# Kernel optimization log

Hardware: AMD Instinct MI355X
Metric: run time of the kernel (lower is better)

## Reference

```python
import jax, jax.numpy as jnp
import numpy as np

B = 8192
I = 1024  # input_size
H = 1024  # hidden_size


def setup_inputs() -> dict:
    key = jax.random.key(0)
    ks = jax.random.split(key, 8)
    s_i = 1.0 / np.sqrt(I)
    s_h = 1.0 / np.sqrt(H)
    return {
        "x": jax.random.normal(ks[0], (B, I), dtype=jnp.float32),
        "h": jax.random.normal(ks[1], (B, H), dtype=jnp.float32),
        # nn.Linear weights have shape [out, in]; y = x @ W.T
        "W_wz": jax.random.uniform(ks[2], (H, I), jnp.float32, -s_i, s_i),
        "W_uz": jax.random.uniform(ks[3], (H, H), jnp.float32, -s_h, s_h),
        "W_wr": jax.random.uniform(ks[4], (H, I), jnp.float32, -s_i, s_i),
        "W_ur": jax.random.uniform(ks[5], (H, H), jnp.float32, -s_h, s_h),
        "W_u": jax.random.uniform(ks[6], (H, H), jnp.float32, -s_h, s_h),
        "W_w": jax.random.uniform(ks[7], (H, I), jnp.float32, -s_i, s_i),
    }


def reference(x, h, W_wz, W_uz, W_wr, W_ur, W_u, W_w):
    # Fuse the three x-projections and the two h-projections into grouped GEMMs.
    # [B, 3H] = x @ [I, 3H]
    xp = x @ jnp.concatenate([W_wz, W_wr, W_w], axis=0).T
    hp = h @ jnp.concatenate([W_uz, W_ur], axis=0).T  # [B, 2H]
    z = jax.nn.sigmoid(xp[:, :H] + hp[:, :H])
    r = jax.nn.sigmoid(xp[:, H:2 * H] + hp[:, H:])
    h_t = jnp.tanh((r * h) @ W_u.T + xp[:, 2 * H:])
    return z * h + (1.0 - z) * h_t
```

## Files before the change

kernel.cpp:

```cpp
#include <hip/hip_runtime.h>

typedef unsigned short u16;
typedef __attribute__((ext_vector_type(8))) short bf16x8;
typedef __attribute__((ext_vector_type(8))) unsigned short u16x8;
typedef __attribute__((ext_vector_type(4))) float f32x4;

__device__ __forceinline__ u16 f2b(float f) {
  unsigned u = __float_as_uint(f);
  u += 0x7FFFu + ((u >> 16) & 1u);
  return (u16)(u >> 16);
}
__device__ __forceinline__ float sigm(float x) { return 1.0f / (1.0f + __expf(-x)); }
__device__ __forceinline__ float tanh_f(float x) { return 1.0f - 2.0f / (__expf(2.0f * x) + 1.0f); }

__device__ __forceinline__ void cp16(const u16* g, u16* l) {
  __builtin_amdgcn_global_load_lds(
      (const __attribute__((address_space(1))) unsigned int*)g,
      (__attribute__((address_space(3))) unsigned int*)l, 16, 0, 0);
}

__device__ __forceinline__ int swz(int b) {
  return b ^ (((b >> 7) & 3) << 5) ^ (((b >> 9) & 1) << 4);
}

__device__ __forceinline__ u16x8 cvt8(float4 a, float4 b) {
  u16x8 v;
  v[0] = f2b(a.x); v[1] = f2b(a.y); v[2] = f2b(a.z); v[3] = f2b(a.w);
  v[4] = f2b(b.x); v[5] = f2b(b.y); v[6] = f2b(b.z); v[7] = f2b(b.w);
  return v;
}

__global__ __launch_bounds__(256) void pack_xh(const float* __restrict__ x,
                                               const float* __restrict__ h,
                                               u16* __restrict__ xhb,
                                               u16* __restrict__ A2) {
  int idx = blockIdx.x * 256 + threadIdx.x;
  int row = idx >> 8;
  int k = (idx & 255) << 3;
  const float* src = (k < 1024) ? (x + (size_t)row * 1024 + k)
                                : (h + (size_t)row * 1024 + (k - 1024));
  float4 a = *reinterpret_cast<const float4*>(src);
  float4 b = *reinterpret_cast<const float4*>(src + 4);
  u16x8 v = cvt8(a, b);
  *reinterpret_cast<u16x8*>(xhb + ((size_t)row << 11) + k) = v;
  if (k < 1024)
    *reinterpret_cast<u16x8*>(A2 + ((size_t)row << 11) + 1024 + k) = v;
}

__global__ __launch_bounds__(256) void pack_W(const float* __restrict__ Wwz,
                                              const float* __restrict__ Wuz,
                                              const float* __restrict__ Wwr,
                                              const float* __restrict__ Wur,
                                              const float* __restrict__ Wu,
                                              const float* __restrict__ Ww,
                                              u16* __restrict__ W1b,
                                              u16* __restrict__ W2b) {
  int idx = blockIdx.x * 256 + threadIdx.x;
  const float* src;
  u16* dst;
  if (idx < 524288) {
    int row = idx >> 8;
    int k = (idx & 255) << 3;
    const float* lo = (row < 1024) ? Wwz : Wwr;
    const float* hi = (row < 1024) ? Wuz : Wur;
    int n = row & 1023;
    src = (k < 1024) ? (lo + (size_t)n * 1024 + k) : (hi + (size_t)n * 1024 + (k - 1024));
    dst = W1b + ((size_t)row << 11) + k;
  } else {
    int j = idx - 524288;
    int row = j >> 8;
    int k = (j & 255) << 3;
    src = (k < 1024) ? (Wu + (size_t)row * 1024 + k) : (Ww + (size_t)row * 1024 + (k - 1024));
    dst = W2b + ((size_t)row << 11) + k;
  }
  float4 a = *reinterpret_cast<const float4*>(src);
  float4 b = *reinterpret_cast<const float4*>(src + 4);
  *reinterpret_cast<u16x8*>(dst) = cvt8(a, b);
}

__device__ __forceinline__ void body(int t, int NT,
                                     const u16* __restrict__ Ag, const u16* __restrict__ Bg,
                                     int lda, int ldb,
                                     const u16* Ar, const u16* Br, u16* Aw, u16* Bw,
                                     int r0, int c2, int arl0, int arl1,
                                     int wr, int wc, int tid, f32x4 acc[4][4]) {
  const int ab = wr * 4096;
  const int bb = wc * 4096;
  bf16x8 af0[2][2], bfr[4][2];
#pragma unroll
  for (int mm = 0; mm < 2; ++mm) {
    af0[mm][0] = *reinterpret_cast<const bf16x8*>(Ar + ab + mm * 1024 + arl0);
    af0[mm][1] = *reinterpret_cast<const bf16x8*>(Ar + ab + mm * 1024 + arl1);
  }
#pragma unroll
  for (int nf = 0; nf < 4; ++nf) {
    bfr[nf][0] = *reinterpret_cast<const bf16x8*>(Br + bb + nf * 1024 + arl0);
    bfr[nf][1] = *reinterpret_cast<const bf16x8*>(Br + bb + nf * 1024 + arl1);
  }
  if (t + 1 < NT) {
    const u16* g0 = Ag + (size_t)r0 * lda + c2 + (size_t)(t + 1) * 64;
    u16* l0 = Aw + tid * 8;
    cp16(g0, l0); cp16(g0 + (size_t)64 * lda, l0 + 4096);
    const u16* g1 = Ag + (size_t)(128 + r0) * lda + c2 + (size_t)(t + 1) * 64;
    u16* l1 = Aw + 8192 + tid * 8;
    cp16(g1, l1); cp16(g1 + (size_t)64 * lda, l1 + 4096);
  }
  __builtin_amdgcn_s_barrier();
  __builtin_amdgcn_s_setprio(1);
#pragma unroll
  for (int mm = 0; mm < 2; ++mm)
#pragma unroll
    for (int nf = 0; nf < 4; ++nf)
#pragma unroll
      for (int ks = 0; ks < 2; ++ks)
        acc[mm][nf] = __builtin_amdgcn_mfma_f32_16x16x32_bf16(
            af0[mm][ks], bfr[nf][ks], acc[mm][nf], 0, 0, 0);
  __builtin_amdgcn_s_setprio(0);
  __builtin_amdgcn_s_barrier();
  bf16x8 af1[2][2];
#pragma unroll
  for (int mm = 0; mm < 2; ++mm) {
    af1[mm][0] = *reinterpret_cast<const bf16x8*>(Ar + ab + (2 + mm) * 1024 + arl0);
    af1[mm][1] = *reinterpret_cast<const bf16x8*>(Ar + ab + (2 + mm) * 1024 + arl1);
  }
  if (t + 2 < NT) {
    const u16* g = Bg + (size_t)r0 * ldb + c2 + (size_t)(t + 2) * 64;
    u16* l = Bw + tid * 8;
    cp16(g, l); cp16(g + (size_t)64 * ldb, l + 4096);
    asm volatile("s_waitcnt vmcnt(2)" ::: "memory");
  } else {
    asm volatile("s_waitcnt vmcnt(0)" ::: "memory");
  }
  __builtin_amdgcn_s_barrier();
  __builtin_amdgcn_s_setprio(1);
#pragma unroll
  for (int mm = 0; mm < 2; ++mm)
#pragma unroll
    for (int nf = 0; nf < 4; ++nf)
#pragma unroll
      for (int ks = 0; ks < 2; ++ks)
        acc[2 + mm][nf] = __builtin_amdgcn_mfma_f32_16x16x32_bf16(
            af1[mm][ks], bfr[nf][ks], acc[2 + mm][nf], 0, 0, 0);
  __builtin_amdgcn_s_setprio(0);
  __builtin_amdgcn_s_barrier();
}

__device__ __forceinline__ void core(const u16* __restrict__ Ag, const u16* __restrict__ Bg,
                                     int lda, int ldb, int NT,
                                     u16* As0, u16* As1, u16* Bs0, u16* Bs1,
                                     f32x4 acc[4][4]) {
  const int tid = threadIdx.x;
  const int lane = tid & 63;
  const int wid = tid >> 6;
  const int wr = wid >> 1;
  const int wc = wid & 1;

  const int plo = tid * 16;
  const int olo = swz(plo);
  const int r0 = olo >> 7;
  const int c2 = (olo & 127) >> 1;

  const int frow = lane & 15;
  const int fcb = (lane >> 4) * 16;
  const int mask = ((frow & 3) << 5) | (((frow >> 2) & 1) << 4);
  const int arl0 = (frow * 128 + ((fcb + 0) ^ mask)) >> 1;
  const int arl1 = (frow * 128 + ((fcb + 64) ^ mask)) >> 1;

  {
    const u16* g; u16* l;
    g = Ag + (size_t)r0 * lda + c2;          l = As0 + tid * 8;        cp16(g, l); cp16(g + (size_t)64 * lda, l + 4096);
    g = Ag + (size_t)(128 + r0) * lda + c2;  l = As0 + 8192 + tid * 8; cp16(g, l); cp16(g + (size_t)64 * lda, l + 4096);
    g = Bg + (size_t)r0 * ldb + c2;          l = Bs0 + tid * 8;        cp16(g, l); cp16(g + (size_t)64 * ldb, l + 4096);
    g = Bg + (size_t)r0 * ldb + c2 + 64;     l = Bs1 + tid * 8;        cp16(g, l); cp16(g + (size_t)64 * ldb, l + 4096);
  }
  asm volatile("s_waitcnt vmcnt(2)" ::: "memory");
  __builtin_amdgcn_s_barrier();

  for (int u = 0; u < NT; u += 2) {
    body(u,     NT, Ag, Bg, lda, ldb, As0, Bs0, As1, Bs0, r0, c2, arl0, arl1, wr, wc, tid, acc);
    body(u + 1, NT, Ag, Bg, lda, ldb, As1, Bs1, As0, Bs1, r0, c2, arl0, arl1, wr, wc, tid, acc);
  }
}

#define CORE_PRE()                                           \
  __shared__ u16 As0[16384];                                 \
  __shared__ u16 As1[16384];                                 \
  __shared__ u16 Bs0[8192];                                  \
  __shared__ u16 Bs1[8192];                                  \
  f32x4 acc[4][4];                                           \
  _Pragma("unroll") for (int m = 0; m < 4; ++m)              \
  _Pragma("unroll") for (int n = 0; n < 4; ++n)              \
      acc[m][n] = (f32x4){0.f, 0.f, 0.f, 0.f};

__global__ __launch_bounds__(512) void gemm_zr(const u16* __restrict__ xhb,
                                               const u16* __restrict__ W1b,
                                               const float* __restrict__ h,
                                               float* __restrict__ zout,
                                               u16* __restrict__ A2) {
  int b = blockIdx.x;
  int wg = (b & 7) * 64 + (b >> 3);
  int mb = wg >> 4, nb = wg & 15;
  const int m0 = mb * 256, n0 = nb * 128;
  CORE_PRE();
  core(xhb + (size_t)m0 * 2048, W1b + (size_t)n0 * 2048, 2048, 2048, 32,
       As0, As1, Bs0, Bs1, acc);

  const int lane = threadIdx.x & 63;
  const int wid = threadIdx.x >> 6;
  const int wr = wid >> 1, wc = wid & 1;
  const int rbase = m0 + wr * 64 + ((lane >> 4) << 2);
  const int cbase = n0 + wc * 64 + (lane & 15);
  const int isz = (n0 < 1024);
#pragma unroll
  for (int m = 0; m < 4; ++m) {
#pragma unroll
    for (int nf = 0; nf < 4; ++nf) {
      const int col = cbase + nf * 16;
#pragma unroll
      for (int j = 0; j < 4; ++j) {
        const int row = rbase + m * 16 + j;
        const float v = acc[m][nf][j];
        if (isz) {
          zout[(size_t)row * 1024 + col] = sigm(v);
        } else {
          const int c = col - 1024;
          const float rh = sigm(v) * h[(size_t)row * 1024 + c];
          A2[((size_t)row << 11) + c] = f2b(rh);
        }
      }
    }
  }
}

__global__ __launch_bounds__(512) void gemm2_k(const u16* __restrict__ A2,
                                               const u16* __restrict__ W2b,
                                               const float* __restrict__ h,
                                               float* __restrict__ out) {
  int b = blockIdx.x;
  int wg = (b & 7) * 32 + (b >> 3);
  int mb = wg >> 3, nb = wg & 7;
  const int m0 = mb * 256, n0 = nb * 128;
  CORE_PRE();
  core(A2 + (size_t)m0 * 2048, W2b + (size_t)n0 * 2048, 2048, 2048, 32,
       As0, As1, Bs0, Bs1, acc);

  const int lane = threadIdx.x & 63;
  const int wid = threadIdx.x >> 6;
  const int wr = wid >> 1, wc = wid & 1;
  const int rbase = m0 + wr * 64 + ((lane >> 4) << 2);
  const int cbase = n0 + wc * 64 + (lane & 15);
#pragma unroll
  for (int m = 0; m < 4; ++m) {
#pragma unroll
    for (int nf = 0; nf < 4; ++nf) {
      const int col = cbase + nf * 16;
#pragma unroll
      for (int j = 0; j < 4; ++j) {
        const int row = rbase + m * 16 + j;
        const size_t idx = (size_t)row * 1024 + col;
        const float z = out[idx];
        const float hv = h[idx];
        const float ht = tanh_f(acc[m][nf][j]);
        out[idx] = z * hv + (1.0f - z) * ht;
      }
    }
  }
}

extern "C" void kernel_launch(void* const* d_in, const int* in_sizes, int n_in,
                              void* d_out, int out_size, void* d_ws, size_t ws_size,
                              hipStream_t stream) {
  const float* x   = (const float*)d_in[0];
  const float* h   = (const float*)d_in[1];
  const float* Wwz = (const float*)d_in[2];
  const float* Wuz = (const float*)d_in[3];
  const float* Wwr = (const float*)d_in[4];
  const float* Wur = (const float*)d_in[5];
  const float* Wu  = (const float*)d_in[6];
  const float* Ww  = (const float*)d_in[7];
  float* out = (float*)d_out;

  char* ws = (char*)d_ws;
  u16* xhb = (u16*)(ws);
  u16* A2  = (u16*)(ws + 33554432);
  u16* W1b = (u16*)(ws + 67108864);
  u16* W2b = (u16*)(ws + 75497472);

  pack_xh<<<8192, 256, 0, stream>>>(x, h, xhb, A2);
  pack_W<<<3072, 256, 0, stream>>>(Wwz, Wuz, Wwr, Wur, Wu, Ww, W1b, W2b);
  gemm_zr<<<512, 512, 0, stream>>>(xhb, W1b, h, out, A2);
  gemm2_k<<<256, 512, 0, stream>>>(A2, W2b, h, out);
}
```

Measured before the change: 313.0 us.

## Replace swizzled 64-wide K pipeline with simple 32-wide double-buffered loop

The hand-scheduled GEMM main loop is replaced. It had XOR-swizzled LDS layout, split A/B prefetch, manual vmcnt waits and setprio. The new loop uses a simple double buffer with 32-element K tiles and __syncthreads. LDS per block is halved and launch bounds request 4 blocks per CU to raise occupancy. In exchange, the unswizzled 64-byte-row LDS layout may cause bank conflicts, and twice as many barriers run per K.

```diff
diff --git a/kernel.cpp b/kernel.cpp
--- a/kernel.cpp
+++ b/kernel.cpp
@@ -17,10 +17,6 @@
   __builtin_amdgcn_global_load_lds(
       (const __attribute__((address_space(1))) unsigned int*)g,
       (__attribute__((address_space(3))) unsigned int*)l, 16, 0, 0);
-}
-
-__device__ __forceinline__ int swz(int b) {
-  return b ^ (((b >> 7) & 3) << 5) ^ (((b >> 9) & 1) << 4);
 }
 
 __device__ __forceinline__ u16x8 cvt8(float4 a, float4 b) {
@@ -78,71 +74,29 @@
   *reinterpret_cast<u16x8*>(dst) = cvt8(a, b);
 }
 
-__device__ __forceinline__ void body(int t, int NT,
-                                     const u16* __restrict__ Ag, const u16* __restrict__ Bg,
-                                     int lda, int ldb,
-                                     const u16* Ar, const u16* Br, u16* Aw, u16* Bw,
-                                     int r0, int c2, int arl0, int arl1,
-                                     int wr, int wc, int tid, f32x4 acc[4][4]) {
-  const int ab = wr * 4096;
-  const int bb = wc * 4096;
-  bf16x8 af0[2][2], bfr[4][2];
-#pragma unroll
-  for (int mm = 0; mm < 2; ++mm) {
-    af0[mm][0] = *reinterpret_cast<const bf16x8*>(Ar + ab + mm * 1024 + arl0);
-    af0[mm][1] = *reinterpret_cast<const bf16x8*>(Ar + ab + mm * 1024 + arl1);
-  }
-#pragma unroll
-  for (int nf = 0; nf < 4; ++nf) {
-    bfr[nf][0] = *reinterpret_cast<const bf16x8*>(Br + bb + nf * 1024 + arl0);
-    bfr[nf][1] = *reinterpret_cast<const bf16x8*>(Br + bb + nf * 1024 + arl1);
-  }
-  if (t + 1 < NT) {
-    const u16* g0 = Ag + (size_t)r0 * lda + c2 + (size_t)(t + 1) * 64;
-    u16* l0 = Aw + tid * 8;
-    cp16(g0, l0); cp16(g0 + (size_t)64 * lda, l0 + 4096);
-    const u16* g1 = Ag + (size_t)(128 + r0) * lda + c2 + (size_t)(t + 1) * 64;
-    u16* l1 = Aw + 8192 + tid * 8;
-    cp16(g1, l1); cp16(g1 + (size_t)64 * lda, l1 + 4096);
-  }
-  __builtin_amdgcn_s_barrier();
-  __builtin_amdgcn_s_setprio(1);
-#pragma unroll
-  for (int mm = 0; mm < 2; ++mm)
-#pragma unroll
-    for (int nf = 0; nf < 4; ++nf)
-#pragma unroll
-      for (int ks = 0; ks < 2; ++ks)
-        acc[mm][nf] = __builtin_amdgcn_mfma_f32_16x16x32_bf16(
-            af0[mm][ks], bfr[nf][ks], acc[mm][nf], 0, 0, 0);
-  __builtin_amdgcn_s_setprio(0);
-  __builtin_amdgcn_s_barrier();
-  bf16x8 af1[2][2];
-#pragma unroll
-  for (int mm = 0; mm < 2; ++mm) {
-    af1[mm][0] = *reinterpret_cast<const bf16x8*>(Ar + ab + (2 + mm) * 1024 + arl0);
-    af1[mm][1] = *reinterpret_cast<const bf16x8*>(Ar + ab + (2 + mm) * 1024 + arl1);
-  }
-  if (t + 2 < NT) {
-    const u16* g = Bg + (size_t)r0 * ldb + c2 + (size_t)(t + 2) * 64;
-    u16* l = Bw + tid * 8;
-    cp16(g, l); cp16(g + (size_t)64 * ldb, l + 4096);
-    asm volatile("s_waitcnt vmcnt(2)" ::: "memory");
-  } else {
-    asm volatile("s_waitcnt vmcnt(0)" ::: "memory");
-  }
-  __builtin_amdgcn_s_barrier();
-  __builtin_amdgcn_s_setprio(1);
-#pragma unroll
-  for (int mm = 0; mm < 2; ++mm)
-#pragma unroll
-    for (int nf = 0; nf < 4; ++nf)
-#pragma unroll
-      for (int ks = 0; ks < 2; ++ks)
-        acc[2 + mm][nf] = __builtin_amdgcn_mfma_f32_16x16x32_bf16(
-            af1[mm][ks], bfr[nf][ks], acc[2 + mm][nf], 0, 0, 0);
-  __builtin_amdgcn_s_setprio(0);
-  __builtin_amdgcn_s_barrier();
+__device__ __forceinline__ void stage_t(const u16* __restrict__ Ag, const u16* __restrict__ Bg,
+                                        int lda, int ldb, int T,
+                                        u16* Abuf, u16* Bbuf, int arow, int acol, int tid) {
+  const u16* ga0 = Ag + (size_t)arow * lda + (size_t)T * 32 + acol;
+  cp16(ga0, Abuf + tid * 8);
+  cp16(ga0 + (size_t)128 * lda, Abuf + 4096 + tid * 8);
+  cp16(Bg + (size_t)arow * ldb + (size_t)T * 32 + acol, Bbuf + tid * 8);
+}
+
+__device__ __forceinline__ void mfma_t(const u16* Ar, const u16* Br,
+                                       int wr, int wc, int fr, int fk, f32x4 acc[4][4]) {
+  bf16x8 af[4], bf[4];
+#pragma unroll
+  for (int m = 0; m < 4; ++m)
+    af[m] = *reinterpret_cast<const bf16x8*>(Ar + (wr * 64 + m * 16 + fr) * 32 + fk);
+#pragma unroll
+  for (int n = 0; n < 4; ++n)
+    bf[n] = *reinterpret_cast<const bf16x8*>(Br + (wc * 64 + n * 16 + fr) * 32 + fk);
+#pragma unroll
+  for (int m = 0; m < 4; ++m)
+#pragma unroll
+    for (int n = 0; n < 4; ++n)
+      acc[m][n] = __builtin_amdgcn_mfma_f32_16x16x32_bf16(af[m], bf[n], acc[m][n], 0, 0, 0);
 }
 
 __device__ __forceinline__ void core(const u16* __restrict__ Ag, const u16* __restrict__ Bg,
@@ -154,55 +108,45 @@
   const int wid = tid >> 6;
   const int wr = wid >> 1;
   const int wc = wid & 1;
-
-  const int plo = tid * 16;
-  const int olo = swz(plo);
-  const int r0 = olo >> 7;
-  const int c2 = (olo & 127) >> 1;
-
-  const int frow = lane & 15;
-  const int fcb = (lane >> 4) * 16;
-  const int mask = ((frow & 3) << 5) | (((frow >> 2) & 1) << 4);
-  const int arl0 = (frow * 128 + ((fcb + 0) ^ mask)) >> 1;
-  const int arl1 = (frow * 128 + ((fcb + 64) ^ mask)) >> 1;
-
-  {
-    const u16* g; u16* l;
-    g = Ag + (size_t)r0 * lda + c2;          l = As0 + tid * 8;        cp16(g, l); cp16(g + (size_t)64 * lda, l + 4096);
-    g = Ag + (size_t)(128 + r0) * lda + c2;  l = As0 + 8192 + tid * 8; cp16(g, l); cp16(g + (size_t)64 * lda, l + 4096);
-    g = Bg + (size_t)r0 * ldb + c2;          l = Bs0 + tid * 8;        cp16(g, l); cp16(g + (size_t)64 * ldb, l + 4096);
-    g = Bg + (size_t)r0 * ldb + c2 + 64;     l = Bs1 + tid * 8;        cp16(g, l); cp16(g + (size_t)64 * ldb, l + 4096);
-  }
-  asm volatile("s_waitcnt vmcnt(2)" ::: "memory");
-  __builtin_amdgcn_s_barrier();
-
-  for (int u = 0; u < NT; u += 2) {
-    body(u,     NT, Ag, Bg, lda, ldb, As0, Bs0, As1, Bs0, r0, c2, arl0, arl1, wr, wc, tid, acc);
-    body(u + 1, NT, Ag, Bg, lda, ldb, As1, Bs1, As0, Bs1, r0, c2, arl0, arl1, wr, wc, tid, acc);
+  const int arow = tid >> 2;
+  const int acol = (tid & 3) * 8;
+  const int fr = lane & 15;
+  const int fk = (lane >> 4) * 8;
+
+  stage_t(Ag, Bg, lda, ldb, 0, As0, Bs0, arow, acol, tid);
+  __syncthreads();
+
+  for (int t = 0; t < NT; t += 2) {
+    if (t + 1 < NT) stage_t(Ag, Bg, lda, ldb, t + 1, As1, Bs1, arow, acol, tid);
+    mfma_t(As0, Bs0, wr, wc, fr, fk, acc);
+    __syncthreads();
+    if (t + 2 < NT) stage_t(Ag, Bg, lda, ldb, t + 2, As0, Bs0, arow, acol, tid);
+    mfma_t(As1, Bs1, wr, wc, fr, fk, acc);
+    __syncthreads();
   }
 }
 
 #define CORE_PRE()                                           \
-  __shared__ u16 As0[16384];                                 \
-  __shared__ u16 As1[16384];                                 \
-  __shared__ u16 Bs0[8192];                                  \
-  __shared__ u16 Bs1[8192];                                  \
+  __shared__ u16 As0[8192];                                  \
+  __shared__ u16 As1[8192];                                  \
+  __shared__ u16 Bs0[4096];                                  \
+  __shared__ u16 Bs1[4096];                                  \
   f32x4 acc[4][4];                                           \
   _Pragma("unroll") for (int m = 0; m < 4; ++m)              \
   _Pragma("unroll") for (int n = 0; n < 4; ++n)              \
       acc[m][n] = (f32x4){0.f, 0.f, 0.f, 0.f};
 
-__global__ __launch_bounds__(512) void gemm_zr(const u16* __restrict__ xhb,
-                                               const u16* __restrict__ W1b,
-                                               const float* __restrict__ h,
-                                               float* __restrict__ zout,
-                                               u16* __restrict__ A2) {
+__global__ __launch_bounds__(512, 4) void gemm_zr(const u16* __restrict__ xhb,
+                                                  const u16* __restrict__ W1b,
+                                                  const float* __restrict__ h,
+                                                  float* __restrict__ zout,
+                                                  u16* __restrict__ A2) {
   int b = blockIdx.x;
   int wg = (b & 7) * 64 + (b >> 3);
   int mb = wg >> 4, nb = wg & 15;
   const int m0 = mb * 256, n0 = nb * 128;
   CORE_PRE();
-  core(xhb + (size_t)m0 * 2048, W1b + (size_t)n0 * 2048, 2048, 2048, 32,
+  core(xhb + (size_t)m0 * 2048, W1b + (size_t)n0 * 2048, 2048, 2048, 64,
        As0, As1, Bs0, Bs1, acc);
 
   const int lane = threadIdx.x & 63;
@@ -232,16 +176,16 @@
   }
 }
 
-__global__ __launch_bounds__(512) void gemm2_k(const u16* __restrict__ A2,
-                                               const u16* __restrict__ W2b,
-                                               const float* __restrict__ h,
-                                               float* __restrict__ out) {
+__global__ __launch_bounds__(512, 4) void gemm2_k(const u16* __restrict__ A2,
+                                                  const u16* __restrict__ W2b,
+                                                  const float* __restrict__ h,
+                                                  float* __restrict__ out) {
   int b = blockIdx.x;
   int wg = (b & 7) * 32 + (b >> 3);
   int mb = wg >> 3, nb = wg & 7;
   const int m0 = mb * 256, n0 = nb * 128;
   CORE_PRE();
-  core(A2 + (size_t)m0 * 2048, W2b + (size_t)n0 * 2048, 2048, 2048, 32,
+  core(A2 + (size_t)m0 * 2048, W2b + (size_t)n0 * 2048, 2048, 2048, 64,
        As0, As1, Bs0, Bs1, acc);
 
   const int lane = threadIdx.x & 63;
```

Measured after the change: 284.7 us. 1.1x faster.
